# Kernel tuning notes

Measured on AMD Instinct MI355X. Metric: run time of the kernel, lower is better.

The kernel has to match this reference:

```python
import jax, jax.numpy as jnp
import numpy as np


def setup_inputs() -> dict:
    key = jax.random.key(0)
    ks = jax.random.split(key, 9)
    B, S, F = 16, 512, 1024
    scale = 1.0 / np.sqrt(2 * F)  # ~torch Linear init scale
    return {
        "v": jax.random.normal(ks[0], (B, S, F), jnp.float32),
        "t": jax.random.normal(ks[1], (B, S, F), jnp.float32),
        "a": jax.random.normal(ks[2], (B, S, F), jnp.float32),
        "W_tv": jax.random.normal(ks[3], (2 * F, F), jnp.float32) * scale,
        "b_tv": jnp.zeros((F,), jnp.float32),
        "W_ta": jax.random.normal(ks[4], (2 * F, F), jnp.float32) * scale,
        "b_ta": jnp.zeros((F,), jnp.float32),
        "W_av": jax.random.normal(ks[5], (2 * F, F), jnp.float32) * scale,
        "b_av": jnp.zeros((F,), jnp.float32),
    }


def _branch_feat(x1, x2, W, b):
    # tanh(Linear(cat(x1, x2)))  -- split weight to avoid materializing concat
    F = x1.shape[-1]
    W1, W2 = W[:F], W[F:]
    return jnp.tanh(jnp.einsum("bsf,fg->bsg", x1, W1)
                    + jnp.einsum("bsf,fg->bsg", x2, W2) + b)


def _attend_gate(q, feat):
    # softmax(q @ feat^T) @ q, gated by feat
    scores = jnp.einsum("bqf,bkf->bqk", q, feat)  # [B,S,S]
    p = jax.nn.softmax(scores, axis=-1)
    return jnp.einsum("bqk,bkf->bqf", p, q) * feat


def reference(v, t, a, W_tv, b_tv, W_ta, b_ta, W_av, b_av):
    Ftv = _branch_feat(t, v, W_tv, b_tv)
    Fta = _branch_feat(t, a, W_ta, b_ta)
    Fav = _branch_feat(a, v, W_av, b_av)
    Oatv = _attend_gate(a, Ftv)
    Ovta = _attend_gate(v, Fta)
    Otav = _attend_gate(t, Fav)
    return jnp.concatenate((Oatv, Ovta, Otav), axis=2)
```

## Files before the change

### kernel.cpp

```cpp
#include <hip/hip_runtime.h>

typedef unsigned short ushort_t;
typedef _Float16 f16x8 __attribute__((ext_vector_type(8)));
typedef float f32x4 __attribute__((ext_vector_type(4)));
typedef unsigned short u16x8 __attribute__((ext_vector_type(8)));

#define DEVINL __device__ __forceinline__

constexpr int B = 16, S = 512, F = 1024;
constexpr int M_ROWS = B * S;
constexpr size_t NX = (size_t)M_ROWS * F;
constexpr size_t NW = (size_t)F * (2 * F);
constexpr size_t NSC = (size_t)3 * B * S * S;

constexpr int XP = 2 * F;

DEVINL ushort_t f2h(float f) { return __builtin_bit_cast(ushort_t, (_Float16)f); }
DEVINL float h2f(ushort_t h) { return (float)__builtin_bit_cast(_Float16, h); }
DEVINL size_t pk(int row, int k, int pitch) {
  return (size_t)row * pitch + ((k >> 5) * 64) + (k & 31);
}

DEVINL void gload_lds16(const void* g, void* l) {
  __builtin_amdgcn_global_load_lds(
      (__attribute__((address_space(1))) void*)(g),
      (__attribute__((address_space(3))) void*)(l), 16, 0, 0);
}

DEVINL f32x4 mfma16h(f16x8 a, f16x8 b, f32x4 c) {
  return __builtin_amdgcn_mfma_f32_16x16x32_f16(a, b, c, 0, 0, 0);
}

template <int KSTEPS, int SPLIT_STEP, bool APACKED>
DEVINL void gemm4p_core(const ushort_t* __restrict__ a1, const ushort_t* __restrict__ a2,
                        int lda, const ushort_t* __restrict__ bsrc, int ldb,
                        ushort_t* lds, int tid, f32x4 (&acc)[4][8]) {
  constexpr int BUF = 32768;
  constexpr int BOFF = 16384;
  constexpr int KM = KSTEPS - 1;
  constexpr int AKC = APACKED ? 128 : 64;
  const int lane = tid & 63, w = tid >> 6;
  const int wr = (w >> 1) * 64, wc = (w & 1) * 128;
  const int slog = (lane & 7) ^ ((lane >> 3) & 7);

  const int sl0 = ((lane >> 4) ^ (lane & 7)) * 8;
  const int sl1 = ((4 + (lane >> 4)) ^ (lane & 7)) * 8;
  const ushort_t* dsA0 = lds + (wr + (lane & 15)) * 64 + sl0;
  const ushort_t* dsA1 = lds + (wr + (lane & 15)) * 64 + sl1;
  const ushort_t* dsB0 = lds + BOFF + (wc + (lane & 15)) * 64 + sl0;
  const ushort_t* dsB1 = lds + BOFF + (wc + (lane & 15)) * 64 + sl1;

  const size_t ldaS = (size_t)lda, ldbS = (size_t)ldb;
  const int colA = APACKED ? ((slog >> 2) * 64 + (slog & 3) * 8) : slog * 8;
  const ushort_t* gA1 = a1 + (size_t)(w * 16 + (lane >> 3)) * ldaS + colA;
  const ushort_t* gA2 = a2 + (size_t)(w * 16 + (lane >> 3)) * ldaS + colA;
  const ushort_t* gB  = bsrc + (size_t)(w * 16 + (lane >> 3)) * ldbS + slog * 8;
  ushort_t* dA = lds + (w * 16) * 64;
  ushort_t* dB = lds + BOFF + (w * 16) * 64;

  auto stA = [&](int bb, int ks, int h) {
    const ushort_t* base = ((SPLIT_STEP >= KSTEPS) || (ks < SPLIT_STEP)) ? gA1 : gA2;
    const ushort_t* s = base + (ks & (SPLIT_STEP - 1)) * AKC + (size_t)(h * 128) * ldaS;
    ushort_t* d = dA + bb * BUF + h * 8192;
    gload_lds16(s, d);
    gload_lds16(s + 8 * ldaS, d + 512);
  };
  auto stB = [&](int bb, int ks, int h) {
    const ushort_t* s = gB + ks * 64 + (size_t)(h * 128) * ldbS;
    ushort_t* d = dB + bb * BUF + h * 8192;
    gload_lds16(s, d);
    gload_lds16(s + 8 * ldbS, d + 512);
  };

#define BAR asm volatile("s_barrier" ::: "memory")
#define RDB(J)                                              \
  Bn0 = *(const f16x8*)(rB0 + (J) * 1024);                  \
  Bn1 = *(const f16x8*)(rB1 + (J) * 1024);                  \
  Bn2 = *(const f16x8*)(rB0 + ((J) + 1) * 1024);            \
  Bn3 = *(const f16x8*)(rB1 + ((J) + 1) * 1024);
#define PHASE_MM(JP)                                        \
  __builtin_amdgcn_s_setprio(1);                            \
  _Pragma("unroll")                                         \
  for (int i = 0; i < 4; ++i) {                             \
    acc[i][2 * (JP)]     = mfma16h(rA[i][0], Bc0, acc[i][2 * (JP)]);     \
    acc[i][2 * (JP)]     = mfma16h(rA[i][1], Bc1, acc[i][2 * (JP)]);     \
    acc[i][2 * (JP) + 1] = mfma16h(rA[i][0], Bc2, acc[i][2 * (JP) + 1]); \
    acc[i][2 * (JP) + 1] = mfma16h(rA[i][1], Bc3, acc[i][2 * (JP) + 1]); \
  }                                                         \
  __builtin_amdgcn_s_setprio(0);
#define SWAPB  Bc0 = Bn0; Bc1 = Bn1; Bc2 = Bn2; Bc3 = Bn3;
#define TILE(BB, T) {                                       \
  const int ksB = ((T) + 1) & KM;                           \
  const int ksA = ((T) + 2) & KM;                           \
  const ushort_t* rA0 = dsA0 + (BB) * BUF;                  \
  const ushort_t* rA1 = dsA1 + (BB) * BUF;                  \
  const ushort_t* rB0 = dsB0 + (BB) * BUF;                  \
  const ushort_t* rB1 = dsB1 + (BB) * BUF;                  \
  f16x8 rA[4][2];                                           \
  f16x8 Bc0, Bc1, Bc2, Bc3, Bn0, Bn1, Bn2, Bn3;             \
  _Pragma("unroll")                                         \
  for (int i = 0; i < 4; ++i) {                             \
    rA[i][0] = *(const f16x8*)(rA0 + i * 1024);             \
    rA[i][1] = *(const f16x8*)(rA1 + i * 1024);             \
  }                                                         \
  Bc0 = *(const f16x8*)(rB0);                               \
  Bc1 = *(const f16x8*)(rB1);                               \
  Bc2 = *(const f16x8*)(rB0 + 1024);                        \
  Bc3 = *(const f16x8*)(rB1 + 1024);                        \
  RDB(2)                                                    \
  stB(BB ^ 1, ksB, 0);                                      \
  BAR; PHASE_MM(0) BAR;                                     \
  SWAPB RDB(4)                                              \
  stB(BB ^ 1, ksB, 1);                                      \
  BAR; PHASE_MM(1) BAR;                                     \
  SWAPB RDB(6)                                              \
  stA(BB, ksA, 0);                                          \
  BAR; PHASE_MM(2) BAR;                                     \
  SWAPB                                                     \
  stA(BB, ksA, 1);                                          \
  BAR; PHASE_MM(3)                                          \
  asm volatile("s_waitcnt vmcnt(4)" ::: "memory");          \
  BAR;                                                      \
}

  stA(0, 0, 0); stA(0, 0, 1);
  stB(0, 0, 0); stB(0, 0, 1);
  stA(1, 1 & KM, 0); stA(1, 1 & KM, 1);
  asm volatile("s_waitcnt vmcnt(4)" ::: "memory");
  BAR;

  for (int t = 0; t < KSTEPS; t += 2) {
    TILE(0, t)
    TILE(1, t + 1)
  }
#undef TILE
#undef SWAPB
#undef PHASE_MM
#undef RDB
#undef BAR
}

template <int KSTEPS, int SPLIT_STEP, int TERMS, int KCHUNK, int NBUF>
DEVINL void gemm_core(const ushort_t* __restrict__ a1, const ushort_t* __restrict__ a2,
                      int lda, const ushort_t* __restrict__ bsrc, int ldb,
                      ushort_t* lds, int tid, f32x4 (&acc)[4][8]) {
  constexpr int BUFE = (TERMS == 2) ? 24576 : 16384;
  constexpr int ALO = 8192;
  constexpr int BOFF = (TERMS == 2) ? 16384 : 8192;
  constexpr int DEPTH = NBUF - 1;
  const int lane = tid & 63, w = tid >> 6;
  const int wr = (w >> 1) * 64, wc = (w & 1) * 128;
  const int scol = (((lane & 3) ^ ((lane >> 3) & 3)) * 8);
  const size_t grow = (size_t)(w * 32 + (lane >> 2));
  const int foff = (lane & 15) * 32 + (((lane >> 4) ^ ((lane >> 1) & 3)) * 8);

  auto stA = [&](int sb, int ks) {
    const ushort_t* base = (ks < SPLIT_STEP) ? a1 : a2;
    int kk = ks & (SPLIT_STEP - 1);
    const ushort_t* s = base + grow * lda + kk * KCHUNK + scol;
    ushort_t* dh = lds + sb * BUFE + w * 1024;
    gload_lds16(s, dh);
    gload_lds16(s + (size_t)16 * lda, dh + 512);
    if constexpr (TERMS == 2) {
      gload_lds16(s + 32, dh + ALO);
      gload_lds16(s + 32 + (size_t)16 * lda, dh + ALO + 512);
    }
  };
  auto stB = [&](int sb, int ks) {
    const ushort_t* s = bsrc + grow * ldb + ks * 32 + scol;
    ushort_t* d = lds + sb * BUFE + BOFF + w * 1024;
    gload_lds16(s, d);
    gload_lds16(s + (size_t)16 * ldb, d + 512);
  };
  auto FR = [&](const ushort_t* rgn, int rb) -> f16x8 {
    return *(const f16x8*)(rgn + rb * 32 + foff);
  };
  auto VMW = [&]() {
    if constexpr (NBUF == 2)       asm volatile("s_waitcnt vmcnt(0)" ::: "memory");
    else if constexpr (TERMS == 2) asm volatile("s_waitcnt vmcnt(6)" ::: "memory");
    else                           asm volatile("s_waitcnt vmcnt(4)" ::: "memory");
  };

#pragma unroll
  for (int d = 0; d < DEPTH; ++d) { stA(d, d); stB(d, d); }
  VMW();
  asm volatile("s_barrier" ::: "memory");

  for (int t = 0; t < KSTEPS; ++t) {
    const int cb = t % NBUF, sb = (t + DEPTH) % NBUF;
    const int ks = (t + DEPTH) & (KSTEPS - 1);
    stA(sb, ks); stB(sb, ks);
    const ushort_t* L = lds + cb * BUFE;
    f16x8 rAh[4], rAl[4], rB[8];
#pragma unroll
    for (int i = 0; i < 4; ++i) rAh[i] = FR(L, wr + i * 16);
#pragma unroll
    for (int j = 0; j < 8; ++j) rB[j] = FR(L + BOFF, wc + j * 16);
    if constexpr (TERMS == 2) {
#pragma unroll
      for (int i = 0; i < 4; ++i) rAl[i] = FR(L + ALO, wr + i * 16);
    }
    __builtin_amdgcn_s_setprio(1);
#pragma unroll
    for (int j = 0; j < 8; ++j)
#pragma unroll
      for (int i = 0; i < 4; ++i) acc[i][j] = mfma16h(rAh[i], rB[j], acc[i][j]);
    if constexpr (TERMS == 2) {
#pragma unroll
      for (int j = 0; j < 8; ++j)
#pragma unroll
        for (int i = 0; i < 4; ++i) acc[i][j] = mfma16h(rAl[i], rB[j], acc[i][j]);
    }
    __builtin_amdgcn_s_setprio(0);
    VMW();
    asm volatile("s_barrier" ::: "memory");
  }
}

__global__ __launch_bounds__(256) void split_x_kernel(
    const float* __restrict__ v, const float* __restrict__ t, const float* __restrict__ a,
    ushort_t* __restrict__ xpack, ushort_t* __restrict__ xT) {
  __shared__ ushort_t tile[64][65];
  int mod = blockIdx.z;
  const float* src = (mod == 0) ? v : (mod == 1 ? t : a);
  int b = blockIdx.y;
  int s0 = (blockIdx.x >> 4) * 64;
  int f0 = (blockIdx.x & 15) * 64;
  int tid = threadIdx.x;
  ushort_t* xp = xpack + mod * (NX * 2);
  ushort_t* xt = xT + mod * NX;
  int fl = (tid & 15) * 4;
#pragma unroll
  for (int r = 0; r < 4; ++r) {
    int sl = (tid >> 4) + r * 16;
    int row = b * S + s0 + sl;
    float4 x = *(const float4*)(src + (size_t)row * F + f0 + fl);
    ushort_t h0 = f2h(x.x), h1 = f2h(x.y), h2 = f2h(x.z), h3 = f2h(x.w);
    size_t o = pk(row, f0 + fl, XP);
    *(ushort4*)(xp + o) = make_ushort4(h0, h1, h2, h3);
    *(ushort4*)(xp + o + 32) = make_ushort4(
        f2h(x.x - h2f(h0)), f2h(x.y - h2f(h1)),
        f2h(x.z - h2f(h2)), f2h(x.w - h2f(h3)));
    tile[sl][fl] = h0; tile[sl][fl + 1] = h1; tile[sl][fl + 2] = h2; tile[sl][fl + 3] = h3;
  }
  __syncthreads();
#pragma unroll
  for (int r = 0; r < 4; ++r) {
    int flr = (tid >> 4) + r * 16;
    int sl4 = (tid & 15) * 4;
    ushort4 o = make_ushort4(tile[sl4][flr], tile[sl4 + 1][flr],
                             tile[sl4 + 2][flr], tile[sl4 + 3][flr]);
    size_t tidx = ((size_t)(b * F + f0 + flr)) * S + s0 + sl4;
    *(ushort4*)(xt + tidx) = o;
  }
}

__global__ __launch_bounds__(256) void split_w_kernel(
    const float* __restrict__ w0, const float* __restrict__ w1, const float* __restrict__ w2,
    ushort_t* __restrict__ wtpack) {
  __shared__ ushort_t th[64][65];
  int br = blockIdx.z;
  const float* w = (br == 0) ? w0 : (br == 1 ? w1 : w2);
  int g0 = blockIdx.x * 64;
  int f0 = blockIdx.y * 64;
  int tid = threadIdx.x;
  int gl = (tid & 15) * 4;
#pragma unroll
  for (int r = 0; r < 4; ++r) {
    int fl = (tid >> 4) + r * 16;
    float4 x = *(const float4*)(w + (size_t)(f0 + fl) * F + g0 + gl);
    th[fl][gl] = f2h(x.x); th[fl][gl + 1] = f2h(x.y);
    th[fl][gl + 2] = f2h(x.z); th[fl][gl + 3] = f2h(x.w);
  }
  __syncthreads();
  ushort_t* op = wtpack + br * NW;
#pragma unroll
  for (int r = 0; r < 4; ++r) {
    int glr = (tid >> 4) + r * 16;
    int fl4 = (tid & 15) * 4;
    size_t o = (size_t)(g0 + glr) * (2 * F) + f0 + fl4;
    *(ushort4*)(op + o) = make_ushort4(th[fl4][glr], th[fl4 + 1][glr],
                                       th[fl4 + 2][glr], th[fl4 + 3][glr]);
  }
}

__global__ __launch_bounds__(512, 2) void feat_gemm_kernel(
    const ushort_t* __restrict__ xpack, const ushort_t* __restrict__ wtpack,
    const float* __restrict__ b0, const float* __restrict__ b1, const float* __restrict__ b2,
    ushort_t* __restrict__ fpack) {
  constexpr int M1[3] = {1, 1, 2};
  constexpr int M2[3] = {0, 2, 0};
  __shared__ __attribute__((aligned(16))) ushort_t lds[2 * 32768];
  int br = blockIdx.z;
  int lin = blockIdx.x;
  int gm0 = ((lin & 7) * 4 + ((lin >> 3) & 3)) * 256;
  int gn0 = (lin >> 5) * 256;
  int tid = threadIdx.x, lane = tid & 63, w = tid >> 6;
  const ushort_t* a1 = xpack + M1[br] * (NX * 2) + (size_t)gm0 * XP;
  const ushort_t* a2 = xpack + M2[br] * (NX * 2) + (size_t)gm0 * XP;
  const ushort_t* bb = wtpack + br * NW + (size_t)gn0 * (2 * F);
  f32x4 acc[4][8] = {};
  gemm4p_core<32, 16, true>(a1, a2, XP, bb, 2 * F, lds, tid, acc);
  const float* bias = (br == 0) ? b0 : (br == 1 ? b1 : b2);
  ushort_t* op = fpack + br * NX;
  int wr = (w >> 1) * 64, wc = (w & 1) * 128;
#pragma unroll
  for (int i = 0; i < 4; ++i)
#pragma unroll
    for (int j = 0; j < 8; ++j)
#pragma unroll
      for (int r = 0; r < 4; ++r) {
        int row = gm0 + wr + i * 16 + (lane >> 4) * 4 + r;
        int col = gn0 + wc + j * 16 + (lane & 15);
        op[(size_t)row * F + col] = f2h(tanhf(acc[i][j][r] + bias[col]));
      }
}

__global__ __launch_bounds__(512, 2) void scores_gemm_kernel(
    const ushort_t* __restrict__ xpack, const ushort_t* __restrict__ fpack,
    float* __restrict__ scores) {
  constexpr int QM[3] = {2, 0, 1};
  __shared__ __attribute__((aligned(16))) ushort_t lds[3 * 24576];
  int z = blockIdx.z;
  int br = z >> 4, b = z & 15;
  int gm0 = blockIdx.x * 256;
  int gn0 = blockIdx.y * 256;
  int tid = threadIdx.x, lane = tid & 63, w = tid >> 6;
  const ushort_t* a1 = xpack + QM[br] * (NX * 2) + (size_t)(b * S + gm0) * XP;
  const ushort_t* bb = fpack + br * NX + (size_t)(b * S + gn0) * F;
  f32x4 acc[4][8] = {};
  gemm_core<32, 32, 2, 64, 3>(a1, a1, XP, bb, F, lds, tid, acc);
  float* out = scores + (size_t)z * S * S;
  int wr = (w >> 1) * 64, wc = (w & 1) * 128;
#pragma unroll
  for (int i = 0; i < 4; ++i)
#pragma unroll
    for (int j = 0; j < 8; ++j)
#pragma unroll
      for (int r = 0; r < 4; ++r) {
        int row = gm0 + wr + i * 16 + (lane >> 4) * 4 + r;
        int col = gn0 + wc + j * 16 + (lane & 15);
        out[(size_t)row * S + col] = acc[i][j][r];
      }
}

__global__ __launch_bounds__(256) void softmax_kernel(
    const float* __restrict__ scores, ushort_t* __restrict__ p) {
  int wave = threadIdx.x >> 6, lane = threadIdx.x & 63;
  int row = blockIdx.x * 4 + wave;
  const float* src = scores + (size_t)row * S;
  float4 v0 = *(const float4*)(src + lane * 8);
  float4 v1 = *(const float4*)(src + lane * 8 + 4);
  float m = fmaxf(fmaxf(fmaxf(v0.x, v0.y), fmaxf(v0.z, v0.w)),
                  fmaxf(fmaxf(v1.x, v1.y), fmaxf(v1.z, v1.w)));
#pragma unroll
  for (int d = 1; d < 64; d <<= 1) m = fmaxf(m, __shfl_xor(m, d));
  float e[8] = {expf(v0.x - m), expf(v0.y - m), expf(v0.z - m), expf(v0.w - m),
                expf(v1.x - m), expf(v1.y - m), expf(v1.z - m), expf(v1.w - m)};
  float s = ((e[0] + e[1]) + (e[2] + e[3])) + ((e[4] + e[5]) + (e[6] + e[7]));
#pragma unroll
  for (int d = 1; d < 64; d <<= 1) s += __shfl_xor(s, d);
  float inv = 1.0f / s;
  u16x8 o;
#pragma unroll
  for (int j = 0; j < 8; ++j) o[j] = f2h(e[j] * inv);
  *(u16x8*)(p + (size_t)row * S + lane * 8) = o;
}

__global__ __launch_bounds__(512, 2) void pv_gemm_kernel(
    const ushort_t* __restrict__ p, const ushort_t* __restrict__ xT,
    const ushort_t* __restrict__ fpack, float* __restrict__ out) {
  constexpr int QM[3] = {2, 0, 1};
  __shared__ __attribute__((aligned(16))) ushort_t lds[2 * 32768];
  int z = blockIdx.z;
  int br = z >> 4, b = z & 15;
  int gm0 = blockIdx.x * 256;
  int gn0 = blockIdx.y * 256;
  int tid = threadIdx.x, lane = tid & 63, w = tid >> 6;
  const ushort_t* pa = p + (size_t)z * S * S + (size_t)gm0 * S;
  const ushort_t* qt = xT + QM[br] * NX + (size_t)b * F * S + (size_t)gn0 * S;
  f32x4 acc[4][8] = {};
  gemm4p_core<8, 8, false>(pa, pa, S, qt, S, lds, tid, acc);
  const ushort_t* fp = fpack + br * NX;
  int wr = (w >> 1) * 64, wc = (w & 1) * 128;
#pragma unroll
  for (int i = 0; i < 4; ++i)
#pragma unroll
    for (int j = 0; j < 8; ++j)
#pragma unroll
      for (int r = 0; r < 4; ++r) {
        int row = gm0 + wr + i * 16 + (lane >> 4) * 4 + r;
        int col = gn0 + wc + j * 16 + (lane & 15);
        float fe = h2f(fp[(size_t)(b * S + row) * F + col]);
        out[(size_t)(b * S + row) * (3 * F) + br * F + col] = acc[i][j][r] * fe;
      }
}

extern "C" void kernel_launch(void* const* d_in, const int* in_sizes, int n_in,
                              void* d_out, int out_size, void* d_ws, size_t ws_size,
                              hipStream_t stream) {
  (void)in_sizes; (void)n_in; (void)out_size; (void)ws_size;
  const float* v = (const float*)d_in[0];
  const float* t = (const float*)d_in[1];
  const float* a = (const float*)d_in[2];
  const float* W_tv = (const float*)d_in[3];
  const float* b_tv = (const float*)d_in[4];
  const float* W_ta = (const float*)d_in[5];
  const float* b_ta = (const float*)d_in[6];
  const float* W_av = (const float*)d_in[7];
  const float* b_av = (const float*)d_in[8];
  float* out = (float*)d_out;

  ushort_t* xpack = (ushort_t*)d_ws;
  ushort_t* xT = xpack + 3 * (NX * 2);
  ushort_t* wtpack = xT + 3 * NX;
  ushort_t* fpack = wtpack + 3 * NW;
  float* scores = (float*)(fpack + 3 * NX);
  ushort_t* pbuf = (ushort_t*)(scores + NSC);

  split_x_kernel<<<dim3(128, 16, 3), 256, 0, stream>>>(v, t, a, xpack, xT);
  split_w_kernel<<<dim3(16, 32, 3), 256, 0, stream>>>(W_tv, W_ta, W_av, wtpack);
  feat_gemm_kernel<<<dim3(128, 1, 3), 512, 0, stream>>>(xpack, wtpack,
                                                        b_tv, b_ta, b_av, fpack);
  scores_gemm_kernel<<<dim3(2, 2, 48), 512, 0, stream>>>(xpack, fpack, scores);
  softmax_kernel<<<dim3((3 * B * S) / 4), 256, 0, stream>>>(scores, pbuf);
  pv_gemm_kernel<<<dim3(2, 4, 48), 512, 0, stream>>>(pbuf, xT, fpack, out);
}
```

Baseline: 333.6 us.

## Drop fp16 hi/lo split of activations, use single-term fp16 GEMMs

Activations were stored as packed fp16 high and low residual halves, and the scores GEMM ran two MFMA terms per step. The change keeps only the fp16 high part in a plain row-major buffer and switches the scores GEMM to the same gemm4p_core used by the other GEMMs. This halves activation-conversion writes and the scores GEMM's MFMA and load work. The cost is lower precision in the scores and feature products, which may affect accuracy against the fp32 reference.

Result: faster. 295.2 us (-11.5%).

```diff
diff --git a/kernel.cpp b/kernel.cpp
--- a/kernel.cpp
+++ b/kernel.cpp
@@ -13,13 +13,8 @@
 constexpr size_t NW = (size_t)F * (2 * F);
 constexpr size_t NSC = (size_t)3 * B * S * S;
 
-constexpr int XP = 2 * F;
-
 DEVINL ushort_t f2h(float f) { return __builtin_bit_cast(ushort_t, (_Float16)f); }
 DEVINL float h2f(ushort_t h) { return (float)__builtin_bit_cast(_Float16, h); }
-DEVINL size_t pk(int row, int k, int pitch) {
-  return (size_t)row * pitch + ((k >> 5) * 64) + (k & 31);
-}
 
 DEVINL void gload_lds16(const void* g, void* l) {
   __builtin_amdgcn_global_load_lds(
@@ -31,14 +26,13 @@
   return __builtin_amdgcn_mfma_f32_16x16x32_f16(a, b, c, 0, 0, 0);
 }
 
-template <int KSTEPS, int SPLIT_STEP, bool APACKED>
+template <int KSTEPS, int SPLIT_STEP>
 DEVINL void gemm4p_core(const ushort_t* __restrict__ a1, const ushort_t* __restrict__ a2,
                         int lda, const ushort_t* __restrict__ bsrc, int ldb,
                         ushort_t* lds, int tid, f32x4 (&acc)[4][8]) {
   constexpr int BUF = 32768;
   constexpr int BOFF = 16384;
   constexpr int KM = KSTEPS - 1;
-  constexpr int AKC = APACKED ? 128 : 64;
   const int lane = tid & 63, w = tid >> 6;
   const int wr = (w >> 1) * 64, wc = (w & 1) * 128;
   const int slog = (lane & 7) ^ ((lane >> 3) & 7);
@@ -51,16 +45,15 @@
   const ushort_t* dsB1 = lds + BOFF + (wc + (lane & 15)) * 64 + sl1;
 
   const size_t ldaS = (size_t)lda, ldbS = (size_t)ldb;
-  const int colA = APACKED ? ((slog >> 2) * 64 + (slog & 3) * 8) : slog * 8;
-  const ushort_t* gA1 = a1 + (size_t)(w * 16 + (lane >> 3)) * ldaS + colA;
-  const ushort_t* gA2 = a2 + (size_t)(w * 16 + (lane >> 3)) * ldaS + colA;
+  const ushort_t* gA1 = a1 + (size_t)(w * 16 + (lane >> 3)) * ldaS + slog * 8;
+  const ushort_t* gA2 = a2 + (size_t)(w * 16 + (lane >> 3)) * ldaS + slog * 8;
   const ushort_t* gB  = bsrc + (size_t)(w * 16 + (lane >> 3)) * ldbS + slog * 8;
   ushort_t* dA = lds + (w * 16) * 64;
   ushort_t* dB = lds + BOFF + (w * 16) * 64;
 
   auto stA = [&](int bb, int ks, int h) {
     const ushort_t* base = ((SPLIT_STEP >= KSTEPS) || (ks < SPLIT_STEP)) ? gA1 : gA2;
-    const ushort_t* s = base + (ks & (SPLIT_STEP - 1)) * AKC + (size_t)(h * 128) * ldaS;
+    const ushort_t* s = base + (ks & (SPLIT_STEP - 1)) * 64 + (size_t)(h * 128) * ldaS;
     ushort_t* d = dA + bb * BUF + h * 8192;
     gload_lds16(s, d);
     gload_lds16(s + 8 * ldaS, d + 512);
@@ -140,86 +133,9 @@
 #undef BAR
 }
 
-template <int KSTEPS, int SPLIT_STEP, int TERMS, int KCHUNK, int NBUF>
-DEVINL void gemm_core(const ushort_t* __restrict__ a1, const ushort_t* __restrict__ a2,
-                      int lda, const ushort_t* __restrict__ bsrc, int ldb,
-                      ushort_t* lds, int tid, f32x4 (&acc)[4][8]) {
-  constexpr int BUFE = (TERMS == 2) ? 24576 : 16384;
-  constexpr int ALO = 8192;
-  constexpr int BOFF = (TERMS == 2) ? 16384 : 8192;
-  constexpr int DEPTH = NBUF - 1;
-  const int lane = tid & 63, w = tid >> 6;
-  const int wr = (w >> 1) * 64, wc = (w & 1) * 128;
-  const int scol = (((lane & 3) ^ ((lane >> 3) & 3)) * 8);
-  const size_t grow = (size_t)(w * 32 + (lane >> 2));
-  const int foff = (lane & 15) * 32 + (((lane >> 4) ^ ((lane >> 1) & 3)) * 8);
-
-  auto stA = [&](int sb, int ks) {
-    const ushort_t* base = (ks < SPLIT_STEP) ? a1 : a2;
-    int kk = ks & (SPLIT_STEP - 1);
-    const ushort_t* s = base + grow * lda + kk * KCHUNK + scol;
-    ushort_t* dh = lds + sb * BUFE + w * 1024;
-    gload_lds16(s, dh);
-    gload_lds16(s + (size_t)16 * lda, dh + 512);
-    if constexpr (TERMS == 2) {
-      gload_lds16(s + 32, dh + ALO);
-      gload_lds16(s + 32 + (size_t)16 * lda, dh + ALO + 512);
-    }
-  };
-  auto stB = [&](int sb, int ks) {
-    const ushort_t* s = bsrc + grow * ldb + ks * 32 + scol;
-    ushort_t* d = lds + sb * BUFE + BOFF + w * 1024;
-    gload_lds16(s, d);
-    gload_lds16(s + (size_t)16 * ldb, d + 512);
-  };
-  auto FR = [&](const ushort_t* rgn, int rb) -> f16x8 {
-    return *(const f16x8*)(rgn + rb * 32 + foff);
-  };
-  auto VMW = [&]() {
-    if constexpr (NBUF == 2)       asm volatile("s_waitcnt vmcnt(0)" ::: "memory");
-    else if constexpr (TERMS == 2) asm volatile("s_waitcnt vmcnt(6)" ::: "memory");
-    else                           asm volatile("s_waitcnt vmcnt(4)" ::: "memory");
-  };
-
-#pragma unroll
-  for (int d = 0; d < DEPTH; ++d) { stA(d, d); stB(d, d); }
-  VMW();
-  asm volatile("s_barrier" ::: "memory");
-
-  for (int t = 0; t < KSTEPS; ++t) {
-    const int cb = t % NBUF, sb = (t + DEPTH) % NBUF;
-    const int ks = (t + DEPTH) & (KSTEPS - 1);
-    stA(sb, ks); stB(sb, ks);
-    const ushort_t* L = lds + cb * BUFE;
-    f16x8 rAh[4], rAl[4], rB[8];
-#pragma unroll
-    for (int i = 0; i < 4; ++i) rAh[i] = FR(L, wr + i * 16);
-#pragma unroll
-    for (int j = 0; j < 8; ++j) rB[j] = FR(L + BOFF, wc + j * 16);
-    if constexpr (TERMS == 2) {
-#pragma unroll
-      for (int i = 0; i < 4; ++i) rAl[i] = FR(L + ALO, wr + i * 16);
-    }
-    __builtin_amdgcn_s_setprio(1);
-#pragma unroll
-    for (int j = 0; j < 8; ++j)
-#pragma unroll
-      for (int i = 0; i < 4; ++i) acc[i][j] = mfma16h(rAh[i], rB[j], acc[i][j]);
-    if constexpr (TERMS == 2) {
-#pragma unroll
-      for (int j = 0; j < 8; ++j)
-#pragma unroll
-        for (int i = 0; i < 4; ++i) acc[i][j] = mfma16h(rAl[i], rB[j], acc[i][j]);
-    }
-    __builtin_amdgcn_s_setprio(0);
-    VMW();
-    asm volatile("s_barrier" ::: "memory");
-  }
-}
-
 __global__ __launch_bounds__(256) void split_x_kernel(
     const float* __restrict__ v, const float* __restrict__ t, const float* __restrict__ a,
-    ushort_t* __restrict__ xpack, ushort_t* __restrict__ xT) {
+    ushort_t* __restrict__ xh, ushort_t* __restrict__ xT) {
   __shared__ ushort_t tile[64][65];
   int mod = blockIdx.z;
   const float* src = (mod == 0) ? v : (mod == 1 ? t : a);
@@ -227,7 +143,7 @@
   int s0 = (blockIdx.x >> 4) * 64;
   int f0 = (blockIdx.x & 15) * 64;
   int tid = threadIdx.x;
-  ushort_t* xp = xpack + mod * (NX * 2);
+  ushort_t* xp = xh + mod * NX;
   ushort_t* xt = xT + mod * NX;
   int fl = (tid & 15) * 4;
 #pragma unroll
@@ -236,11 +152,7 @@
     int row = b * S + s0 + sl;
     float4 x = *(const float4*)(src + (size_t)row * F + f0 + fl);
     ushort_t h0 = f2h(x.x), h1 = f2h(x.y), h2 = f2h(x.z), h3 = f2h(x.w);
-    size_t o = pk(row, f0 + fl, XP);
-    *(ushort4*)(xp + o) = make_ushort4(h0, h1, h2, h3);
-    *(ushort4*)(xp + o + 32) = make_ushort4(
-        f2h(x.x - h2f(h0)), f2h(x.y - h2f(h1)),
-        f2h(x.z - h2f(h2)), f2h(x.w - h2f(h3)));
+    *(ushort4*)(xp + (size_t)row * F + f0 + fl) = make_ushort4(h0, h1, h2, h3);
     tile[sl][fl] = h0; tile[sl][fl + 1] = h1; tile[sl][fl + 2] = h2; tile[sl][fl + 3] = h3;
   }
   __syncthreads();
@@ -285,7 +197,7 @@
 }
 
 __global__ __launch_bounds__(512, 2) void feat_gemm_kernel(
-    const ushort_t* __restrict__ xpack, const ushort_t* __restrict__ wtpack,
+    const ushort_t* __restrict__ xh, const ushort_t* __restrict__ wtpack,
     const float* __restrict__ b0, const float* __restrict__ b1, const float* __restrict__ b2,
     ushort_t* __restrict__ fpack) {
   constexpr int M1[3] = {1, 1, 2};
@@ -296,11 +208,11 @@
   int gm0 = ((lin & 7) * 4 + ((lin >> 3) & 3)) * 256;
   int gn0 = (lin >> 5) * 256;
   int tid = threadIdx.x, lane = tid & 63, w = tid >> 6;
-  const ushort_t* a1 = xpack + M1[br] * (NX * 2) + (size_t)gm0 * XP;
-  const ushort_t* a2 = xpack + M2[br] * (NX * 2) + (size_t)gm0 * XP;
+  const ushort_t* a1 = xh + M1[br] * NX + (size_t)gm0 * F;
+  const ushort_t* a2 = xh + M2[br] * NX + (size_t)gm0 * F;
   const ushort_t* bb = wtpack + br * NW + (size_t)gn0 * (2 * F);
   f32x4 acc[4][8] = {};
-  gemm4p_core<32, 16, true>(a1, a2, XP, bb, 2 * F, lds, tid, acc);
+  gemm4p_core<32, 16>(a1, a2, F, bb, 2 * F, lds, tid, acc);
   const float* bias = (br == 0) ? b0 : (br == 1 ? b1 : b2);
   ushort_t* op = fpack + br * NX;
   int wr = (w >> 1) * 64, wc = (w & 1) * 128;
@@ -317,19 +229,19 @@
 }
 
 __global__ __launch_bounds__(512, 2) void scores_gemm_kernel(
-    const ushort_t* __restrict__ xpack, const ushort_t* __restrict__ fpack,
+    const ushort_t* __restrict__ xh, const ushort_t* __restrict__ fpack,
     float* __restrict__ scores) {
   constexpr int QM[3] = {2, 0, 1};
-  __shared__ __attribute__((aligned(16))) ushort_t lds[3 * 24576];
+  __shared__ __attribute__((aligned(16))) ushort_t lds[2 * 32768];
   int z = blockIdx.z;
   int br = z >> 4, b = z & 15;
   int gm0 = blockIdx.x * 256;
   int gn0 = blockIdx.y * 256;
   int tid = threadIdx.x, lane = tid & 63, w = tid >> 6;
-  const ushort_t* a1 = xpack + QM[br] * (NX * 2) + (size_t)(b * S + gm0) * XP;
+  const ushort_t* a1 = xh + QM[br] * NX + (size_t)(b * S + gm0) * F;
   const ushort_t* bb = fpack + br * NX + (size_t)(b * S + gn0) * F;
   f32x4 acc[4][8] = {};
-  gemm_core<32, 32, 2, 64, 3>(a1, a1, XP, bb, F, lds, tid, acc);
+  gemm4p_core<16, 16>(a1, a1, F, bb, F, lds, tid, acc);
   float* out = scores + (size_t)z * S * S;
   int wr = (w >> 1) * 64, wc = (w & 1) * 128;
 #pragma unroll
@@ -380,7 +292,7 @@
   const ushort_t* pa = p + (size_t)z * S * S + (size_t)gm0 * S;
   const ushort_t* qt = xT + QM[br] * NX + (size_t)b * F * S + (size_t)gn0 * S;
   f32x4 acc[4][8] = {};
-  gemm4p_core<8, 8, false>(pa, pa, S, qt, S, lds, tid, acc);
+  gemm4p_core<8, 8>(pa, pa, S, qt, S, lds, tid, acc);
   const ushort_t* fp = fpack + br * NX;
   int wr = (w >> 1) * 64, wc = (w & 1) * 128;
 #pragma unroll
@@ -411,18 +323,18 @@
   const float* b_av = (const float*)d_in[8];
   float* out = (float*)d_out;
 
-  ushort_t* xpack = (ushort_t*)d_ws;
-  ushort_t* xT = xpack + 3 * (NX * 2);
+  ushort_t* xh = (ushort_t*)d_ws;
+  ushort_t* xT = xh + 3 * NX;
   ushort_t* wtpack = xT + 3 * NX;
   ushort_t* fpack = wtpack + 3 * NW;
   float* scores = (float*)(fpack + 3 * NX);
   ushort_t* pbuf = (ushort_t*)(scores + NSC);
 
-  split_x_kernel<<<dim3(128, 16, 3), 256, 0, stream>>>(v, t, a, xpack, xT);
+  split_x_kernel<<<dim3(128, 16, 3), 256, 0, stream>>>(v, t, a, xh, xT);
   split_w_kernel<<<dim3(16, 32, 3), 256, 0, stream>>>(W_tv, W_ta, W_av, wtpack);
-  feat_gemm_kernel<<<dim3(128, 1, 3), 512, 0, stream>>>(xpack, wtpack,
+  feat_gemm_kernel<<<dim3(128, 1, 3), 512, 0, stream>>>(xh, wtpack,
                                                         b_tv, b_ta, b_av, fpack);
-  scores_gemm_kernel<<<dim3(2, 2, 48), 512, 0, stream>>>(xpack, fpack, scores);
+  scores_gemm_kernel<<<dim3(2, 2, 48), 512, 0, stream>>>(xh, fpack, scores);
   softmax_kernel<<<dim3((3 * B * S) / 4), 256, 0, stream>>>(scores, pbuf);
   pv_gemm_kernel<<<dim3(2, 4, 48), 512, 0, stream>>>(pbuf, xT, fpack, out);
 }
```
